# Kernel optimization log

Measured on AMD Instinct MI355X. Metric: run time of the kernel, lower is better.

## Reference

```python
import jax, jax.numpy as jnp
import numpy as np

B, L, E = 4, 2048, 1024
H, D = 16, 64  # heads, head_dim; H*D == E


def setup_inputs() -> dict:
    key = jax.random.key(0)
    ks = jax.random.split(key, 6)
    s = 0.02
    return {
        "x": jax.random.normal(ks[0], (B, L, E), dtype=jnp.float32),
        "Wq": jax.random.normal(ks[1], (E, H * D), dtype=jnp.float32) * s,
        "Wk": jax.random.normal(ks[2], (E, H * D), dtype=jnp.float32) * s,
        "Wv": jax.random.normal(ks[3], (E, H * D), dtype=jnp.float32) * s,
        "Wo": jax.random.normal(ks[4], (H * D, E), dtype=jnp.float32) * s,
        "bo": jax.random.normal(ks[5], (E,), dtype=jnp.float32) * s,
    }


def reference(x, Wq, Wk, Wv, Wo, bo):
    b, l, e = x.shape
    q = (x @ Wq).reshape(b, l, H, D)
    k = (x @ Wk).reshape(b, l, H, D)
    v = (x @ Wv).reshape(b, l, H, D)
    # NOTE: original scales by sqrt(embed_size), not sqrt(head_dim)
    energy = jnp.einsum('nqhd,nkhd->nhqk', q, k)
    attn = jax.nn.softmax(energy / jnp.sqrt(jnp.float32(e)), axis=3)
    out = jnp.einsum('nhql,nlhd->nqhd', attn, v).reshape(b, l, H * D)
    return out @ Wo + bo
```

## Files before the change

### kernel.cpp

```cpp
#include <hip/hip_runtime.h>

#define B_ 4
#define L_ 2048
#define E_ 1024
#define H_ 16
#define D_ 64
#define CSCALE 0.045084960222629414f

typedef short s16x8 __attribute__((ext_vector_type(8)));
typedef short s16x4 __attribute__((ext_vector_type(4)));
typedef float f32x4 __attribute__((ext_vector_type(4)));

__device__ __forceinline__ unsigned short f2bf(float f) {
  union { float f; unsigned int u; } v;
  v.f = f;
  unsigned int u = v.u;
  u += 0x7fffu + ((u >> 16) & 1u);
  return (unsigned short)(u >> 16);
}

__device__ __forceinline__ unsigned short f2bf_pos(float f) {
  union { float f; unsigned int u; } v;
  v.f = f;
  return (unsigned short)((v.u + 0x8000u) >> 16);
}

__device__ __forceinline__ void async16(const void* g, void* l) {
  __builtin_amdgcn_global_load_lds(
      (__attribute__((address_space(1))) void*)(g),
      (__attribute__((address_space(3))) void*)(l), 16, 0, 0);
}

__global__ void k_prep(const float* __restrict__ x,
                       const float* __restrict__ Wq, const float* __restrict__ Wk,
                       const float* __restrict__ Wv, const float* __restrict__ Wo,
                       unsigned short* __restrict__ xb,
                       unsigned short* __restrict__ Wt, unsigned short* __restrict__ WoT) {
  __shared__ float t[32][33];
  int bid = blockIdx.x, tid = threadIdx.x;
  if (bid < 8192) {
    int i = bid * 256 + tid;
    float4 v = ((const float4*)x)[i];
    ushort4 o;
    o.x = f2bf(v.x); o.y = f2bf(v.y); o.z = f2bf(v.z); o.w = f2bf(v.w);
    ((ushort4*)xb)[i] = o;
    return;
  }
  int tt = bid - 8192;
  int wsel = tt >> 10, tile = tt & 1023;
  const float* in = (wsel == 0) ? Wq : (wsel == 1) ? Wk : (wsel == 2) ? Wv : Wo;
  unsigned short* out = (wsel == 0) ? Wt : (wsel == 1) ? Wt + (1u << 20)
                        : (wsel == 2) ? Wt + (2u << 20) : WoT;
  int bx = tile & 31, by = tile >> 5;
  int tx = tid & 31, ty = tid >> 5;
  int xcol = bx * 32 + tx;
  int y0 = by * 32;
#pragma unroll
  for (int i = 0; i < 4; ++i)
    t[ty + i * 8][tx] = in[(size_t)(y0 + ty + i * 8) * 1024 + xcol];
  __syncthreads();
  int xo = by * 32 + tx;
  int yo0 = bx * 32;
#pragma unroll
  for (int i = 0; i < 4; ++i)
    out[(size_t)(yo0 + ty + i * 8) * 1024 + xo] = f2bf(t[tx][ty + i * 8]);
}

__global__ __launch_bounds__(256) void k_gemm_qkvt(
    const unsigned short* __restrict__ xb, const unsigned short* __restrict__ Wt,
    unsigned short* __restrict__ Qb, unsigned short* __restrict__ Kb,
    unsigned short* __restrict__ Vt) {
  __shared__ __align__(16) unsigned short As[128 * 32];
  __shared__ __align__(16) unsigned short Bs[128 * 32];
  const int bid = blockIdx.x;
  const int tid = threadIdx.x;
  const int w = tid >> 6, lane = tid & 63;
  const int quad = lane >> 4, mrow = lane & 15;
  const bool isQK = bid < 1024;
  int m0, n0;
  const unsigned short *PA, *PB;
  if (isQK) {
    m0 = (bid & 63) * 128;
    n0 = (bid >> 6) * 128;
    PA = xb + (size_t)m0 * 1024;
    PB = Wt + (size_t)n0 * 1024;
  } else {
    int g = bid - 1024;
    m0 = (g & 7) * 128;
    n0 = (g >> 3) * 128;
    PA = Wt + (2u << 20) + (size_t)m0 * 1024;
    PB = xb + (size_t)n0 * 1024;
  }
  const int wr = (w >> 1) * 64, wc = (w & 1) * 64;
  const f32x4 fz = {0.f, 0.f, 0.f, 0.f};
  f32x4 acc[4][4];
#pragma unroll
  for (int a = 0; a < 4; ++a)
#pragma unroll
    for (int b = 0; b < 4; ++b) acc[a][b] = fz;

  for (int kt = 0; kt < 32; ++kt) {
    __syncthreads();
#pragma unroll
    for (int r = 0; r < 2; ++r) {
      int c = r * 256 + tid;
      int row = c >> 2, cc = c & 3;
      async16(PA + (size_t)row * 1024 + kt * 32 + cc * 8, &As[c * 8]);
    }
#pragma unroll
    for (int r = 0; r < 2; ++r) {
      int c = r * 256 + tid;
      int row = c >> 2, cc = c & 3;
      async16(PB + (size_t)row * 1024 + kt * 32 + cc * 8, &Bs[c * 8]);
    }
    __syncthreads();
    s16x8 a[4], b[4];
#pragma unroll
    for (int mt = 0; mt < 4; ++mt)
      a[mt] = *(const s16x8*)&As[(wr + mt * 16 + mrow) * 32 + quad * 8];
#pragma unroll
    for (int nt = 0; nt < 4; ++nt)
      b[nt] = *(const s16x8*)&Bs[(wc + nt * 16 + mrow) * 32 + quad * 8];
#pragma unroll
    for (int mt = 0; mt < 4; ++mt)
#pragma unroll
      for (int nt = 0; nt < 4; ++nt)
        acc[mt][nt] = __builtin_amdgcn_mfma_f32_16x16x32_bf16(a[mt], b[nt], acc[mt][nt], 0, 0, 0);
  }
  if (isQK) {
#pragma unroll
    for (int mt = 0; mt < 4; ++mt)
#pragma unroll
      for (int nt = 0; nt < 4; ++nt)
#pragma unroll
        for (int i = 0; i < 4; ++i) {
          int row = m0 + wr + mt * 16 + quad * 4 + i;
          int col = n0 + wc + nt * 16 + mrow;
          int bb = row >> 11, l = row & 2047;
          if (col < 1024) {
            int h = col >> 6, d = col & 63;
            Qb[(((size_t)(bb * 16 + h)) * 2048 + l) * 64 + d] = f2bf(acc[mt][nt][i]);
          } else {
            int c2 = col - 1024, h = c2 >> 6, d = c2 & 63;
            Kb[(((size_t)(bb * 16 + h)) * 2048 + l) * 64 + d] = f2bf(acc[mt][nt][i] * CSCALE);
          }
        }
  } else {
#pragma unroll
    for (int mt = 0; mt < 4; ++mt)
#pragma unroll
      for (int nt = 0; nt < 4; ++nt)
#pragma unroll
        for (int i = 0; i < 4; ++i) {
          int f = m0 + wr + mt * 16 + quad * 4 + i;
          int tk = n0 + wc + nt * 16 + mrow;
          int bb = tk >> 11, l = tk & 2047;
          Vt[((size_t)(bb * 1024 + f)) * 2048 + l] = f2bf(acc[mt][nt][i]);
        }
  }
}

__global__ __launch_bounds__(256, 2) void k_attn(
    const unsigned short* __restrict__ Qb, const unsigned short* __restrict__ Kb,
    const unsigned short* __restrict__ Vt, unsigned short* __restrict__ AO) {
  __shared__ __align__(16) unsigned short KVs[2][8192];
  const int tid = threadIdx.x, w = tid >> 6, lane = tid & 63;
  const int quad = lane >> 4, mrow = lane & 15;
  const int bh = blockIdx.y;
  const int q0 = blockIdx.x * 256;
  const unsigned short* Qh = Qb + (size_t)bh * 2048 * 64;
  const unsigned short* Kh = Kb + (size_t)bh * 2048 * 64;
  const unsigned short* Vh = Vt + (size_t)bh * 64 * 2048;
  unsigned short* KVf = &KVs[0][0];

#pragma unroll
  for (int r = 0; r < 8; ++r) {
    int c = r * 256 + tid;
    int row = c >> 3, cl = c & 7;
    int gc = cl ^ (row & 7);
    async16(Qh + (size_t)(q0 + row) * 64 + gc * 8, &KVf[c * 8]);
  }
  __syncthreads();
  s16x8 qb[4][2];
#pragma unroll
  for (int nt = 0; nt < 4; ++nt)
#pragma unroll
    for (int ks = 0; ks < 2; ++ks) {
      int row = w * 64 + nt * 16 + mrow;
      qb[nt][ks] = *(const s16x8*)&KVf[row * 64 + (((ks * 4 + quad) ^ (row & 7)) << 3)];
    }
  __syncthreads();

#pragma unroll
  for (int r = 0; r < 2; ++r) {
    int c = r * 256 + tid;
    int row = c >> 3, cl = c & 7;
    int gc = cl ^ (row & 7);
    async16(Kh + (size_t)row * 64 + gc * 8, &KVs[0][c * 8]);
  }
#pragma unroll
  for (int r = 0; r < 2; ++r) {
    int c = r * 256 + tid;
    int row = c >> 3, cl = c & 7;
    int gc = cl ^ (row & 7);
    async16(Vh + (size_t)row * 2048 + gc * 8, &KVs[0][4096 + c * 8]);
  }

  const f32x4 fz = {0.f, 0.f, 0.f, 0.f};
  f32x4 o[4][4];
  float lr[4];
#pragma unroll
  for (int nt = 0; nt < 4; ++nt) {
    lr[nt] = 0.f;
#pragma unroll
    for (int dt = 0; dt < 4; ++dt) o[nt][dt] = fz;
  }

  for (int j = 0; j < 32; ++j) {
    __syncthreads();
    const unsigned short* Kt = &KVs[j & 1][0];
    const unsigned short* Vs = &KVs[j & 1][4096];

    s16x8 ak[4][2];
#pragma unroll
    for (int mt = 0; mt < 4; ++mt)
#pragma unroll
      for (int ks = 0; ks < 2; ++ks) {
        int row = mt * 16 + mrow;
        ak[mt][ks] = *(const s16x8*)&Kt[row * 64 + (((ks * 4 + quad) ^ (row & 7)) << 3)];
      }
    s16x4 vb[4][4];
#pragma unroll
    for (int dt = 0; dt < 4; ++dt)
#pragma unroll
      for (int lt = 0; lt < 4; ++lt) {
        int row = dt * 16 + mrow;
        int lbase = lt * 16 + quad * 4;
        int cg = lbase >> 3, off = lbase & 7;
        vb[dt][lt] = *(const s16x4*)&Vs[row * 64 + ((cg ^ (row & 7)) << 3) + off];
      }

    if (j + 1 < 32) {
      unsigned short* nb = &KVs[(j + 1) & 1][0];
#pragma unroll
      for (int r = 0; r < 2; ++r) {
        int c = r * 256 + tid;
        int row = c >> 3, cl = c & 7;
        int gc = cl ^ (row & 7);
        async16(Kh + (size_t)((j + 1) * 64 + row) * 64 + gc * 8, &nb[c * 8]);
      }
#pragma unroll
      for (int r = 0; r < 2; ++r) {
        int c = r * 256 + tid;
        int row = c >> 3, cl = c & 7;
        int gc = cl ^ (row & 7);
        async16(Vh + (size_t)row * 2048 + (j + 1) * 64 + gc * 8, &nb[4096 + c * 8]);
      }
    }

    f32x4 s[4][4];
#pragma unroll
    for (int mt = 0; mt < 4; ++mt)
#pragma unroll
      for (int nt = 0; nt < 4; ++nt) s[mt][nt] = fz;
#pragma unroll
    for (int ks = 0; ks < 2; ++ks)
#pragma unroll
      for (int mt = 0; mt < 4; ++mt)
#pragma unroll
        for (int nt = 0; nt < 4; ++nt)
          s[mt][nt] = __builtin_amdgcn_mfma_f32_16x16x32_bf16(ak[mt][ks], qb[nt][ks], s[mt][nt], 0, 0, 0);

    s16x4 pa[4][4];
#pragma unroll
    for (int mt = 0; mt < 4; ++mt)
#pragma unroll
      for (int nt = 0; nt < 4; ++nt) {
        float p0 = __builtin_amdgcn_exp2f(s[mt][nt][0]);
        float p1 = __builtin_amdgcn_exp2f(s[mt][nt][1]);
        float p2 = __builtin_amdgcn_exp2f(s[mt][nt][2]);
        float p3 = __builtin_amdgcn_exp2f(s[mt][nt][3]);
        lr[nt] += (p0 + p1) + (p2 + p3);
        s16x4 pk;
        pk[0] = (short)f2bf_pos(p0);
        pk[1] = (short)f2bf_pos(p1);
        pk[2] = (short)f2bf_pos(p2);
        pk[3] = (short)f2bf_pos(p3);
        pa[mt][nt] = pk;
      }

#pragma unroll
    for (int nt = 0; nt < 4; ++nt)
#pragma unroll
      for (int dt = 0; dt < 4; ++dt)
#pragma unroll
        for (int lt = 0; lt < 4; ++lt)
          o[nt][dt] = __builtin_amdgcn_mfma_f32_16x16x16bf16_1k(pa[lt][nt], vb[dt][lt], o[nt][dt], 0, 0, 0);
  }

#pragma unroll
  for (int nt = 0; nt < 4; ++nt) {
    float v = lr[nt];
    v += __shfl_xor(v, 16);
    v += __shfl_xor(v, 32);
    lr[nt] = v;
  }

  int b_ = bh >> 4, h = bh & 15;
#pragma unroll
  for (int nt = 0; nt < 4; ++nt)
#pragma unroll
    for (int i = 0; i < 4; ++i) {
      float inv = 1.f / __shfl(lr[nt], quad * 4 + i, 64);
      int qrow = q0 + w * 64 + nt * 16 + quad * 4 + i;
#pragma unroll
      for (int dt = 0; dt < 4; ++dt) {
        int d = dt * 16 + mrow;
        AO[((size_t)(b_ * 2048 + qrow)) * 1024 + h * 64 + d] = f2bf(o[nt][dt][i] * inv);
      }
    }
}

__global__ __launch_bounds__(256) void k_gemm_out(
    const unsigned short* __restrict__ Ab, const unsigned short* __restrict__ WoT,
    const float* __restrict__ bo, float* __restrict__ out) {
  __shared__ __align__(16) unsigned short As[128 * 32];
  __shared__ __align__(16) unsigned short Bs[128 * 32];
  const int tid = threadIdx.x;
  const int w = tid >> 6, lane = tid & 63;
  const int quad = lane >> 4, mrow = lane & 15;
  const int m0 = blockIdx.x * 128, n0 = blockIdx.y * 128;
  const int wr = (w >> 1) * 64, wc = (w & 1) * 64;
  const f32x4 fz = {0.f, 0.f, 0.f, 0.f};
  f32x4 acc[4][4];
#pragma unroll
  for (int a = 0; a < 4; ++a)
#pragma unroll
    for (int b = 0; b < 4; ++b) acc[a][b] = fz;

  for (int kt = 0; kt < 32; ++kt) {
    __syncthreads();
#pragma unroll
    for (int r = 0; r < 2; ++r) {
      int c = r * 256 + tid;
      int row = c >> 2, cc = c & 3;
      async16(Ab + (size_t)(m0 + row) * 1024 + kt * 32 + cc * 8, &As[c * 8]);
    }
#pragma unroll
    for (int r = 0; r < 2; ++r) {
      int c = r * 256 + tid;
      int row = c >> 2, cc = c & 3;
      async16(WoT + (size_t)(n0 + row) * 1024 + kt * 32 + cc * 8, &Bs[c * 8]);
    }
    __syncthreads();
    s16x8 a[4], b[4];
#pragma unroll
    for (int mt = 0; mt < 4; ++mt)
      a[mt] = *(const s16x8*)&As[(wr + mt * 16 + mrow) * 32 + quad * 8];
#pragma unroll
    for (int nt = 0; nt < 4; ++nt)
      b[nt] = *(const s16x8*)&Bs[(wc + nt * 16 + mrow) * 32 + quad * 8];
#pragma unroll
    for (int mt = 0; mt < 4; ++mt)
#pragma unroll
      for (int nt = 0; nt < 4; ++nt)
        acc[mt][nt] = __builtin_amdgcn_mfma_f32_16x16x32_bf16(a[mt], b[nt], acc[mt][nt], 0, 0, 0);
  }
#pragma unroll
  for (int mt = 0; mt < 4; ++mt)
#pragma unroll
    for (int nt = 0; nt < 4; ++nt)
#pragma unroll
      for (int i = 0; i < 4; ++i) {
        int row = m0 + wr + mt * 16 + quad * 4 + i;
        int col = n0 + wc + nt * 16 + mrow;
        out[(size_t)row * 1024 + col] = acc[mt][nt][i] + bo[col];
      }
}

extern "C" void kernel_launch(void* const* d_in, const int* in_sizes, int n_in,
                              void* d_out, int out_size, void* d_ws, size_t ws_size,
                              hipStream_t stream) {
  const float* x  = (const float*)d_in[0];
  const float* Wq = (const float*)d_in[1];
  const float* Wk = (const float*)d_in[2];
  const float* Wv = (const float*)d_in[3];
  const float* Wo = (const float*)d_in[4];
  const float* bo = (const float*)d_in[5];
  float* out = (float*)d_out;

  char* ws = (char*)d_ws;
  const size_t MiB = 1u << 20;
  unsigned short* xb  = (unsigned short*)(ws);
  unsigned short* Wt  = (unsigned short*)(ws + 16 * MiB);
  unsigned short* WoT = (unsigned short*)(ws + 22 * MiB);
  unsigned short* Qb  = (unsigned short*)(ws + 24 * MiB);
  unsigned short* Kb  = (unsigned short*)(ws + 40 * MiB);
  unsigned short* Vt  = (unsigned short*)(ws + 56 * MiB);
  unsigned short* AO  = xb;

  k_prep<<<12288, 256, 0, stream>>>(x, Wq, Wk, Wv, Wo, xb, Wt, WoT);
  k_gemm_qkvt<<<1536, 256, 0, stream>>>(xb, Wt, Qb, Kb, Vt);
  k_attn<<<dim3(8, 64), 256, 0, stream>>>(Qb, Kb, Vt, AO);
  k_gemm_out<<<dim3(64, 8), 256, 0, stream>>>(AO, WoT, bo, out);
}
```

Measured before the change: 280.2 us.

## Split attention block across eight waves with setprio and packed bf16 conversion

The attention kernel now runs 512 threads per block, so each of eight waves owns 32 query rows instead of 64. The K/V tile loads are spread over more threads, and the per-wave accumulator and score register footprint is halved, which allows higher occupancy (launch bounds 512,4). MFMA sections are wrapped in s_setprio to favour matrix issue, and the manual round-half-up bf16 packing is replaced by the hardware v_cvt_pk_bf16_f32 instruction. The trade-off is that each wave now reloads the full K/V fragments from LDS for half as much compute, which raises LDS read traffic per FLOP.

```diff
diff --git a/kernel.cpp b/kernel.cpp
--- a/kernel.cpp
+++ b/kernel.cpp
@@ -17,12 +17,6 @@
   unsigned int u = v.u;
   u += 0x7fffu + ((u >> 16) & 1u);
   return (unsigned short)(u >> 16);
-}
-
-__device__ __forceinline__ unsigned short f2bf_pos(float f) {
-  union { float f; unsigned int u; } v;
-  v.f = f;
-  return (unsigned short)((v.u + 0x8000u) >> 16);
 }
 
 __device__ __forceinline__ void async16(const void* g, void* l) {
@@ -160,7 +154,7 @@
   }
 }
 
-__global__ __launch_bounds__(256, 2) void k_attn(
+__global__ __launch_bounds__(512, 4) void k_attn(
     const unsigned short* __restrict__ Qb, const unsigned short* __restrict__ Kb,
     const unsigned short* __restrict__ Vt, unsigned short* __restrict__ AO) {
   __shared__ __align__(16) unsigned short KVs[2][8192];
@@ -174,43 +168,36 @@
   unsigned short* KVf = &KVs[0][0];
 
 #pragma unroll
-  for (int r = 0; r < 8; ++r) {
-    int c = r * 256 + tid;
+  for (int r = 0; r < 4; ++r) {
+    int c = r * 512 + tid;
     int row = c >> 3, cl = c & 7;
     int gc = cl ^ (row & 7);
     async16(Qh + (size_t)(q0 + row) * 64 + gc * 8, &KVf[c * 8]);
   }
   __syncthreads();
-  s16x8 qb[4][2];
-#pragma unroll
-  for (int nt = 0; nt < 4; ++nt)
+  s16x8 qb[2][2];
+#pragma unroll
+  for (int nt = 0; nt < 2; ++nt)
 #pragma unroll
     for (int ks = 0; ks < 2; ++ks) {
-      int row = w * 64 + nt * 16 + mrow;
+      int row = w * 32 + nt * 16 + mrow;
       qb[nt][ks] = *(const s16x8*)&KVf[row * 64 + (((ks * 4 + quad) ^ (row & 7)) << 3)];
     }
   __syncthreads();
 
-#pragma unroll
-  for (int r = 0; r < 2; ++r) {
-    int c = r * 256 + tid;
+  {
+    int c = tid;
     int row = c >> 3, cl = c & 7;
     int gc = cl ^ (row & 7);
     async16(Kh + (size_t)row * 64 + gc * 8, &KVs[0][c * 8]);
-  }
-#pragma unroll
-  for (int r = 0; r < 2; ++r) {
-    int c = r * 256 + tid;
-    int row = c >> 3, cl = c & 7;
-    int gc = cl ^ (row & 7);
     async16(Vh + (size_t)row * 2048 + gc * 8, &KVs[0][4096 + c * 8]);
   }
 
   const f32x4 fz = {0.f, 0.f, 0.f, 0.f};
-  f32x4 o[4][4];
-  float lr[4];
-#pragma unroll
-  for (int nt = 0; nt < 4; ++nt) {
+  f32x4 o[2][4];
+  float lr[2];
+#pragma unroll
+  for (int nt = 0; nt < 2; ++nt) {
     lr[nt] = 0.f;
 #pragma unroll
     for (int dt = 0; dt < 4; ++dt) o[nt][dt] = fz;
@@ -242,64 +229,59 @@
 
     if (j + 1 < 32) {
       unsigned short* nb = &KVs[(j + 1) & 1][0];
-#pragma unroll
-      for (int r = 0; r < 2; ++r) {
-        int c = r * 256 + tid;
-        int row = c >> 3, cl = c & 7;
-        int gc = cl ^ (row & 7);
-        async16(Kh + (size_t)((j + 1) * 64 + row) * 64 + gc * 8, &nb[c * 8]);
-      }
-#pragma unroll
-      for (int r = 0; r < 2; ++r) {
-        int c = r * 256 + tid;
-        int row = c >> 3, cl = c & 7;
-        int gc = cl ^ (row & 7);
-        async16(Vh + (size_t)row * 2048 + (j + 1) * 64 + gc * 8, &nb[4096 + c * 8]);
-      }
-    }
-
-    f32x4 s[4][4];
-#pragma unroll
-    for (int mt = 0; mt < 4; ++mt)
-#pragma unroll
-      for (int nt = 0; nt < 4; ++nt) s[mt][nt] = fz;
+      int c = tid;
+      int row = c >> 3, cl = c & 7;
+      int gc = cl ^ (row & 7);
+      async16(Kh + (size_t)((j + 1) * 64 + row) * 64 + gc * 8, &nb[c * 8]);
+      async16(Vh + (size_t)row * 2048 + (j + 1) * 64 + gc * 8, &nb[4096 + c * 8]);
+    }
+
+    f32x4 s[4][2];
+#pragma unroll
+    for (int mt = 0; mt < 4; ++mt)
+#pragma unroll
+      for (int nt = 0; nt < 2; ++nt) s[mt][nt] = fz;
+    __builtin_amdgcn_s_setprio(1);
 #pragma unroll
     for (int ks = 0; ks < 2; ++ks)
 #pragma unroll
       for (int mt = 0; mt < 4; ++mt)
 #pragma unroll
-        for (int nt = 0; nt < 4; ++nt)
+        for (int nt = 0; nt < 2; ++nt)
           s[mt][nt] = __builtin_amdgcn_mfma_f32_16x16x32_bf16(ak[mt][ks], qb[nt][ks], s[mt][nt], 0, 0, 0);
-
-    s16x4 pa[4][4];
-#pragma unroll
-    for (int mt = 0; mt < 4; ++mt)
-#pragma unroll
-      for (int nt = 0; nt < 4; ++nt) {
+    __builtin_amdgcn_s_setprio(0);
+
+    s16x4 pa[4][2];
+#pragma unroll
+    for (int mt = 0; mt < 4; ++mt)
+#pragma unroll
+      for (int nt = 0; nt < 2; ++nt) {
         float p0 = __builtin_amdgcn_exp2f(s[mt][nt][0]);
         float p1 = __builtin_amdgcn_exp2f(s[mt][nt][1]);
         float p2 = __builtin_amdgcn_exp2f(s[mt][nt][2]);
         float p3 = __builtin_amdgcn_exp2f(s[mt][nt][3]);
         lr[nt] += (p0 + p1) + (p2 + p3);
-        s16x4 pk;
-        pk[0] = (short)f2bf_pos(p0);
-        pk[1] = (short)f2bf_pos(p1);
-        pk[2] = (short)f2bf_pos(p2);
-        pk[3] = (short)f2bf_pos(p3);
-        pa[mt][nt] = pk;
-      }
-
-#pragma unroll
-    for (int nt = 0; nt < 4; ++nt)
+        unsigned int r01, r23;
+        asm("v_cvt_pk_bf16_f32 %0, %1, %2" : "=v"(r01) : "v"(p0), "v"(p1));
+        asm("v_cvt_pk_bf16_f32 %0, %1, %2" : "=v"(r23) : "v"(p2), "v"(p3));
+        union { unsigned int u[2]; s16x4 v4; } uu;
+        uu.u[0] = r01; uu.u[1] = r23;
+        pa[mt][nt] = uu.v4;
+      }
+
+    __builtin_amdgcn_s_setprio(1);
+#pragma unroll
+    for (int nt = 0; nt < 2; ++nt)
 #pragma unroll
       for (int dt = 0; dt < 4; ++dt)
 #pragma unroll
         for (int lt = 0; lt < 4; ++lt)
           o[nt][dt] = __builtin_amdgcn_mfma_f32_16x16x16bf16_1k(pa[lt][nt], vb[dt][lt], o[nt][dt], 0, 0, 0);
-  }
-
-#pragma unroll
-  for (int nt = 0; nt < 4; ++nt) {
+    __builtin_amdgcn_s_setprio(0);
+  }
+
+#pragma unroll
+  for (int nt = 0; nt < 2; ++nt) {
     float v = lr[nt];
     v += __shfl_xor(v, 16);
     v += __shfl_xor(v, 32);
@@ -308,11 +290,11 @@
 
   int b_ = bh >> 4, h = bh & 15;
 #pragma unroll
-  for (int nt = 0; nt < 4; ++nt)
+  for (int nt = 0; nt < 2; ++nt)
 #pragma unroll
     for (int i = 0; i < 4; ++i) {
       float inv = 1.f / __shfl(lr[nt], quad * 4 + i, 64);
-      int qrow = q0 + w * 64 + nt * 16 + quad * 4 + i;
+      int qrow = q0 + w * 32 + nt * 16 + quad * 4 + i;
 #pragma unroll
       for (int dt = 0; dt < 4; ++dt) {
         int d = dt * 16 + mrow;
@@ -401,6 +383,6 @@
 
   k_prep<<<12288, 256, 0, stream>>>(x, Wq, Wk, Wv, Wo, xb, Wt, WoT);
   k_gemm_qkvt<<<1536, 256, 0, stream>>>(xb, Wt, Qb, Kb, Vt);
-  k_attn<<<dim3(8, 64), 256, 0, stream>>>(Qb, Kb, Vt, AO);
+  k_attn<<<dim3(8, 64), 512, 0, stream>>>(Qb, Kb, Vt, AO);
   k_gemm_out<<<dim3(64, 8), 256, 0, stream>>>(AO, WoT, bo, out);
 }
```

Measured after the change: 319.3 us. +14.0%, slower.
